# Kernel optimization log

Hardware: AMD Instinct MI355X
Metric: run time of the kernel (lower is better)

The kernel has to match this reference:

```python
import jax, jax.numpy as jnp
import numpy as np

B, T, D, H, L = 256, 128, 32, 512, 6
EPS = 1e-5


def setup_inputs() -> dict:
    key = jax.random.key(0)
    ks = jax.random.split(key, 12)
    sc = 0.02
    rn = lambda k, shp, s: (jax.random.normal(k, shp, jnp.float32) * s)
    return {
        "x": rn(ks[0], (B, T, D), 1.0),
        "w_proj": rn(ks[1], (H, D), sc),
        "b_proj": jnp.zeros((H,), jnp.float32),
        "w_ih": rn(ks[2], (L, 4 * H, H), sc),
        "w_hh": rn(ks[3], (L, 4 * H, H), sc),
        "b_ih": jnp.zeros((L, 4 * H), jnp.float32),
        "b_hh": jnp.zeros((L, 4 * H), jnp.float32),
        "ln_g": jnp.ones((L, H), jnp.float32),
        "ln_b": jnp.zeros((L, H), jnp.float32),
        "w1": rn(ks[4], (H, H), sc),
        "b1": jnp.zeros((H,), jnp.float32),
        "w2": rn(ks[5], (H // 2, H), sc),
        "b2": jnp.zeros((H // 2,), jnp.float32),
        "w3": rn(ks[6], (1, H // 2), sc),
        "b3": jnp.zeros((1,), jnp.float32),
    }


def _layer_norm(x, g, b):
    mu = jnp.mean(x, axis=-1, keepdims=True)
    var = jnp.mean(jnp.square(x - mu), axis=-1, keepdims=True)
    return (x - mu) * jax.lax.rsqrt(var + EPS) * g + b


def _lstm_layer(x, wih, whh, bih, bhh):
    # Precompute input-gate contributions for the whole sequence: [B,T,4H]
    xg = jnp.einsum("bth,gh->btg", x, wih) + (bih + bhh)
    h0 = jnp.zeros((x.shape[0], whh.shape[1]), x.dtype)

    def step(carry, xg_t):
        h, c = carry
        gates = xg_t + h @ whh.T  # [B,4H], torch gate order i,f,g,o
        i, f, g, o = jnp.split(gates, 4, axis=-1)
        i = jax.nn.sigmoid(i)
        f = jax.nn.sigmoid(f)
        g = jnp.tanh(g)
        o = jax.nn.sigmoid(o)
        c = f * c + i * g
        h = o * jnp.tanh(c)
        return (h, c), h

    _, hs = jax.lax.scan(step, (h0, h0), jnp.swapaxes(xg, 0, 1))  # hs: [T,B,H]
    return jnp.swapaxes(hs, 0, 1)  # [B,T,H]


def reference(x, w_proj, b_proj, w_ih, w_hh, b_ih, b_hh, ln_g, ln_b,
              w1, b1, w2, b2, w3, b3):
    h_prev = x @ w_proj.T + b_proj  # input projection: [B,T,H]
    for i in range(L):
        out = _lstm_layer(h_prev, w_ih[i], w_hh[i], b_ih[i], b_hh[i])
        out = _layer_norm(out, ln_g[i], ln_b[i])
        # dropout is identity in eval mode
        if i > 0:
            out = out + h_prev
        h_prev = out
    last = out[:, -1, :]  # [B,H]
    z = jax.nn.relu(last @ w1.T + b1)
    z = jax.nn.relu(z @ w2.T + b2)
    return z @ w3.T + b3  # [B,1]
```

## Files before the change

### kernel.cpp

```cpp
#include <hip/hip_runtime.h>
#include <hip/hip_bf16.h>
#include <stdint.h>

#define BB 256
#define TT 128
#define DD 32
#define HH 512
#define NL 6

typedef __attribute__((ext_vector_type(8))) short short8;
typedef __attribute__((ext_vector_type(4))) float f32x4;

__device__ __forceinline__ unsigned short f2bf(float f) {
    union { float f; unsigned u; } v; v.f = f;
    unsigned r = v.u + 0x7fff + ((v.u >> 16) & 1);
    return (unsigned short)(r >> 16);
}
__device__ __forceinline__ float bf2f(unsigned short s) {
    union { unsigned u; float f; } v; v.u = ((unsigned)s) << 16;
    return v.f;
}
__device__ __forceinline__ float fsig(float x) { return 1.0f / (1.0f + __expf(-x)); }
__device__ __forceinline__ float ftanh(float x) {
    float e = __expf(-2.0f * fabsf(x));
    float t = (1.0f - e) / (1.0f + e);
    return x < 0.0f ? -t : t;
}

__device__ __forceinline__ int4 g_load16_cc(const void* p) {
    int4 r;
    asm volatile("global_load_dwordx4 %0, %1, off sc0 sc1" : "=v"(r) : "v"(p) : "memory");
    return r;
}
__device__ __forceinline__ void g_store16_cc(void* p, int4 v) {
    union { int4 q; unsigned long long d[2]; } u; u.q = v;
    void* p2 = (void*)((char*)p + 8);
    asm volatile("global_store_dwordx2 %0, %1, off sc0 sc1" :: "v"(p), "v"(u.d[0]) : "memory");
    asm volatile("global_store_dwordx2 %0, %1, off sc0 sc1" :: "v"(p2), "v"(u.d[1]) : "memory");
}

__device__ __forceinline__ void poll_ge(unsigned int* p, unsigned target) {
    int guard = 0;
    while (__hip_atomic_load(p, __ATOMIC_RELAXED, __HIP_MEMORY_SCOPE_AGENT) < target &&
           ++guard < (1 << 17)) {}
}

__global__ __launch_bounds__(256) void k_zero(unsigned int* __restrict__ p, int n) {
    int i = blockIdx.x * 256 + threadIdx.x;
    if (i < n) p[i] = 0;
}

__global__ __launch_bounds__(256) void k_convert(const float* __restrict__ wih, const float* __restrict__ whh,
                                                 unsigned short* __restrict__ wih_bf, unsigned short* __restrict__ whh_bf,
                                                 int n4) {
    int i = blockIdx.x * 256 + threadIdx.x;
    if (i >= n4) return;
    float4 a = ((const float4*)wih)[i];
    float4 b = ((const float4*)whh)[i];
    ushort4 ra; ra.x = f2bf(a.x); ra.y = f2bf(a.y); ra.z = f2bf(a.z); ra.w = f2bf(a.w);
    ushort4 rb; rb.x = f2bf(b.x); rb.y = f2bf(b.y); rb.z = f2bf(b.z); rb.w = f2bf(b.w);
    ((ushort4*)wih_bf)[i] = ra;
    ((ushort4*)whh_bf)[i] = rb;
}

__global__ __launch_bounds__(512) void k_proj(const float* __restrict__ x, const float* __restrict__ wp,
                                              const float* __restrict__ bp,
                                              unsigned short* __restrict__ abf) {
    __shared__ float xs[64][DD];
    int m0 = blockIdx.x * 64;
    for (int i = threadIdx.x; i < 64 * DD; i += 512)
        xs[i >> 5][i & 31] = x[(size_t)(m0 + (i >> 5)) * DD + (i & 31)];
    __syncthreads();
    int n = threadIdx.x;
    float w[DD];
#pragma unroll
    for (int k = 0; k < DD; k++) w[k] = wp[n * DD + k];
    float bias = bp[n];
    for (int r = 0; r < 64; r++) {
        float acc = bias;
#pragma unroll
        for (int k = 0; k < DD; k++) acc += xs[r][k] * w[k];
        abf[(size_t)(m0 + r) * HH + n] = f2bf(acc);
    }
}

__device__ __forceinline__ void do_ln(int l, int tln, int row, int li, bool final_out,
                                      const unsigned short* __restrict__ hbuf,
                                      unsigned short* __restrict__ xring,
                                      const float* __restrict__ ln_g, const float* __restrict__ ln_b,
                                      float* __restrict__ xfinal) {
    const unsigned short* hrow = hbuf + ((size_t)(l * 2 + (tln & 1))) * 131072 + (size_t)row * 512 + li * 16;
    int4 h0 = g_load16_cc(hrow);
    int4 h1 = g_load16_cc(hrow + 8);
    int4 r0, r1;
    const bool res = (l > 0);
    if (res) {
        const unsigned short* xrow = xring + ((size_t)((l - 1) * 16 + (tln & 15))) * 131072 + (size_t)row * 512 + li * 16;
        r0 = g_load16_cc(xrow);
        r1 = g_load16_cc(xrow + 8);
    }
    asm volatile("s_waitcnt vmcnt(0)" ::: "memory");
    __builtin_amdgcn_sched_barrier(0);
    const unsigned short* hu0 = (const unsigned short*)&h0;
    const unsigned short* hu1 = (const unsigned short*)&h1;
    float v[16];
    float s = 0.f, ss = 0.f;
#pragma unroll
    for (int e = 0; e < 8; e++) { v[e] = bf2f(hu0[e]); v[e + 8] = bf2f(hu1[e]); }
#pragma unroll
    for (int e = 0; e < 16; e++) { s += v[e]; ss += v[e] * v[e]; }
#pragma unroll
    for (int off = 1; off < 32; off <<= 1) {
        s += __shfl_xor(s, off);
        ss += __shfl_xor(ss, off);
    }
    float mu = s * (1.f / 512.f);
    float var = ss * (1.f / 512.f) - mu * mu;
    float rs = rsqrtf(var + 1e-5f);
    const unsigned short* ru0 = (const unsigned short*)&r0;
    const unsigned short* ru1 = (const unsigned short*)&r1;
    float y[16];
#pragma unroll
    for (int e = 0; e < 16; e++) {
        float yy = (v[e] - mu) * rs * ln_g[l * 512 + li * 16 + e] + ln_b[l * 512 + li * 16 + e];
        if (res) yy += bf2f(e < 8 ? ru0[e] : ru1[e - 8]);
        y[e] = yy;
    }
    if (final_out) {
        float* dst = xfinal + (size_t)row * 512 + li * 16;
#pragma unroll
        for (int q = 0; q < 4; q++)
            *(float4*)(dst + q * 4) = (float4){y[q * 4], y[q * 4 + 1], y[q * 4 + 2], y[q * 4 + 3]};
    } else {
        unsigned short ys[16];
#pragma unroll
        for (int e = 0; e < 16; e++) ys[e] = f2bf(y[e]);
        unsigned short* dst = xring + ((size_t)(l * 16 + (tln & 15))) * 131072 + (size_t)row * 512 + li * 16;
        g_store16_cc(dst, *(int4*)&ys[0]);
        g_store16_cc(dst + 8, *(int4*)&ys[8]);
    }
}

__global__ __launch_bounds__(256, 1) void k_mega(
    const unsigned short* __restrict__ wih_bf,
    const unsigned short* __restrict__ whh_bf,
    const unsigned short* __restrict__ a_bf,
    const float* __restrict__ bih_all, const float* __restrict__ bhh_all,
    const float* __restrict__ ln_g, const float* __restrict__ ln_b,
    unsigned short* __restrict__ xring,
    unsigned short* __restrict__ hbuf,
    float* __restrict__ xfinal,
    unsigned int* __restrict__ cnt)
{
    __shared__ unsigned short smem[128 * 512];
    __shared__ unsigned short hstage[128 * 40];

    const int blk = blockIdx.x;
    const int l = blk >> 5;
    const int rr_ = blk & 31;
    const int g = rr_ >> 4;
    const int ui = rr_ & 15;
    const int tid = threadIdx.x, lane = tid & 63, w = tid >> 6;
    const int u0 = ui * 32;
    const int gb0 = g * 128;
    const int wb0 = gb0 + w * 32;
    const int uu = lane & 15;
    const int kg = lane >> 4;

    const unsigned short* wih = wih_bf + (size_t)l * 2048 * 512;
    const unsigned short* whh = whh_bf + (size_t)l * 2048 * 512;
    unsigned int* c1  = cnt + (l * 2 + g) * 64;
    unsigned int* c1n = cnt + ((l + 1) * 2 + g) * 64;
    unsigned int* c2  = cnt + (12 + l * 2 + g) * 64;
    unsigned int* c2u = cnt + (12 + (l - 1) * 2 + g) * 64;

    for (int c = tid; c < 128 * 64; c += 256) {
        int rr = c >> 6, k16 = c & 63;
        int grow = (rr >> 5) * 512 + u0 + ((rr >> 4) & 1) * 16 + (rr & 15);
        int4 v = *(const int4*)(whh + (size_t)grow * 512 + k16 * 8);
        int baddr = (rr * 1024 + k16 * 16) ^ ((rr & 7) << 4);
        *(int4*)((char*)smem + baddr) = v;
    }
    __syncthreads();

    float biasg[8];
#pragma unroll
    for (int rt = 0; rt < 8; rt++) {
        int grow = (rt >> 1) * 512 + u0 + ((rt & 1) << 4) + uu;
        biasg[rt] = bih_all[l * 2048 + grow] + bhh_all[l * 2048 + grow];
    }

    const int ln_row = gb0 + ui * 8 + w * 2 + (lane >> 5);
    const int li = lane & 31;
    f32x4 cst[4];
#pragma unroll
    for (int q = 0; q < 4; q++) cst[q] = (f32x4){0.f, 0.f, 0.f, 0.f};

#pragma unroll 1
    for (int t = 0; t < TT; ++t) {
        if (tid == 0) {
            if (t > 0) poll_ge(c1, 16u * (unsigned)t);
            if (l < 5 && t >= 17) poll_ge(c1n, 16u * (unsigned)(t - 15));
        }
        __syncthreads();

        if (t > 0 && l < 5) {
            do_ln(l, t - 1, ln_row, li, false, hbuf, xring, ln_g, ln_b, xfinal);
            asm volatile("s_waitcnt vmcnt(0)" ::: "memory");
            __syncthreads();
            if (tid == 0)
                __hip_atomic_fetch_add(c2, 1u, __ATOMIC_RELAXED, __HIP_MEMORY_SCOPE_AGENT);
        }

        if (l > 0) {
            if (tid == 0) poll_ge(c2u, 16u * (unsigned)(t + 1));
            __syncthreads();
        }

        f32x4 acc[2][8];
#pragma unroll
        for (int bt = 0; bt < 2; bt++)
#pragma unroll
            for (int rt = 0; rt < 8; rt++)
                acc[bt][rt] = (f32x4){biasg[rt], biasg[rt], biasg[rt], biasg[rt]};

#pragma unroll
        for (int half = 0; half < 2; half++) {
            short8 ax[2][8];
            if (l == 0) {
#pragma unroll
                for (int bt = 0; bt < 2; bt++)
#pragma unroll
                    for (int k8 = 0; k8 < 8; k8++)
                        ax[bt][k8] = *(const short8*)(a_bf + ((size_t)(wb0 + bt * 16 + uu) * TT + t) * 512 +
                                                      (half * 8 + k8) * 32 + kg * 8);
            } else {
                const unsigned short* xs = xring + ((size_t)((l - 1) * 16 + (t & 15))) * 131072;
                int4 ai[2][8];
#pragma unroll
                for (int bt = 0; bt < 2; bt++)
#pragma unroll
                    for (int k8 = 0; k8 < 8; k8++)
                        ai[bt][k8] = g_load16_cc(xs + (size_t)(wb0 + bt * 16 + uu) * 512 +
                                                 (half * 8 + k8) * 32 + kg * 8);
                asm volatile("s_waitcnt vmcnt(0)" ::: "memory");
                __builtin_amdgcn_sched_barrier(0);
#pragma unroll
                for (int bt = 0; bt < 2; bt++)
#pragma unroll
                    for (int k8 = 0; k8 < 8; k8++)
                        ax[bt][k8] = *(short8*)&ai[bt][k8];
            }
#pragma unroll
            for (int k8 = 0; k8 < 8; k8++) {
                int ks = half * 8 + k8;
#pragma unroll
                for (int rt = 0; rt < 8; rt++) {
                    short8 bfr = *(const short8*)(wih + (size_t)((rt >> 1) * 512 + u0 + ((rt & 1) << 4) + uu) * 512 +
                                                  ks * 32 + kg * 8);
                    acc[0][rt] = __builtin_amdgcn_mfma_f32_16x16x32_bf16(ax[0][k8], bfr, acc[0][rt], 0, 0, 0);
                    acc[1][rt] = __builtin_amdgcn_mfma_f32_16x16x32_bf16(ax[1][k8], bfr, acc[1][rt], 0, 0, 0);
                }
            }
        }

        if (t > 0) {
            const unsigned short* hp = hbuf + ((size_t)(l * 2 + ((t - 1) & 1))) * 131072;
#pragma unroll
            for (int half = 0; half < 2; half++) {
                int4 ai[2][8];
#pragma unroll
                for (int bt = 0; bt < 2; bt++)
#pragma unroll
                    for (int k8 = 0; k8 < 8; k8++)
                        ai[bt][k8] = g_load16_cc(hp + (size_t)(wb0 + bt * 16 + uu) * 512 +
                                                 (half * 8 + k8) * 32 + kg * 8);
                asm volatile("s_waitcnt vmcnt(0)" ::: "memory");
                __builtin_amdgcn_sched_barrier(0);
#pragma unroll
                for (int k8 = 0; k8 < 8; k8++) {
                    int k2 = ((half * 8 + k8) * 32 + kg * 8) * 2;
                    short8 ah0 = *(short8*)&ai[0][k8];
                    short8 ah1 = *(short8*)&ai[1][k8];
#pragma unroll
                    for (int rt = 0; rt < 8; rt++) {
                        int rr = rt * 16 + uu;
                        int baddr = (rr * 1024 + k2) ^ ((rr & 7) << 4);
                        short8 bh = *(const short8*)((const char*)smem + baddr);
                        acc[0][rt] = __builtin_amdgcn_mfma_f32_16x16x32_bf16(ah0, bh, acc[0][rt], 0, 0, 0);
                        acc[1][rt] = __builtin_amdgcn_mfma_f32_16x16x32_bf16(ah1, bh, acc[1][rt], 0, 0, 0);
                    }
                }
            }
        }

#pragma unroll
        for (int bt = 0; bt < 2; bt++)
#pragma unroll
            for (int usub = 0; usub < 2; usub++) {
                f32x4 iq = acc[bt][0 + usub], fq = acc[bt][2 + usub];
                f32x4 gq = acc[bt][4 + usub], oq = acc[bt][6 + usub];
#pragma unroll
                for (int j = 0; j < 4; j++) {
                    float i_ = fsig(iq[j]);
                    float f_ = fsig(fq[j]);
                    float g_ = ftanh(gq[j]);
                    float o_ = fsig(oq[j]);
                    float c = f_ * cst[bt * 2 + usub][j] + i_ * g_;
                    cst[bt * 2 + usub][j] = c;
                    float h = o_ * ftanh(c);
                    hstage[(w * 32 + bt * 16 + kg * 4 + j) * 40 + usub * 16 + uu] = f2bf(h);
                }
            }
        __syncthreads();
        {
            int lb = tid >> 1, hf = tid & 1;
            int4 v0 = *(const int4*)(hstage + lb * 40 + hf * 16);
            int4 v1 = *(const int4*)(hstage + lb * 40 + hf * 16 + 8);
            unsigned short* hd = hbuf + ((size_t)(l * 2 + (t & 1))) * 131072 + (size_t)(gb0 + lb) * 512 + u0 + hf * 16;
            g_store16_cc(hd, v0);
            g_store16_cc(hd + 8, v1);
        }
        asm volatile("s_waitcnt vmcnt(0)" ::: "memory");
        __syncthreads();
        if (tid == 0)
            __hip_atomic_fetch_add(c1, 1u, __ATOMIC_RELAXED, __HIP_MEMORY_SCOPE_AGENT);
    }

    if (tid == 0) poll_ge(c1, 16u * 128u);
    __syncthreads();
    if (l < 5) {
        do_ln(l, TT - 1, ln_row, li, false, hbuf, xring, ln_g, ln_b, xfinal);
        asm volatile("s_waitcnt vmcnt(0)" ::: "memory");
        __syncthreads();
        if (tid == 0)
            __hip_atomic_fetch_add(c2, 1u, __ATOMIC_RELAXED, __HIP_MEMORY_SCOPE_AGENT);
    } else {
        do_ln(l, TT - 1, ln_row, li, true, hbuf, xring, ln_g, ln_b, xfinal);
    }
}

__global__ __launch_bounds__(512) void k_mlp1(const float* __restrict__ xfinal, const float* __restrict__ w1,
                                              const float* __restrict__ b1, float* __restrict__ z1) {
    __shared__ float xs[512];
    int b = blockIdx.x;
    xs[threadIdx.x] = xfinal[(size_t)b * 512 + threadIdx.x];
    __syncthreads();
    int n = threadIdx.x;
    const float4* wr = (const float4*)(w1 + (size_t)n * 512);
    float acc = b1[n];
#pragma unroll 4
    for (int k4 = 0; k4 < 128; k4++) {
        float4 wv = wr[k4];
        acc += xs[k4 * 4 + 0] * wv.x + xs[k4 * 4 + 1] * wv.y + xs[k4 * 4 + 2] * wv.z + xs[k4 * 4 + 3] * wv.w;
    }
    z1[(size_t)b * 512 + n] = fmaxf(acc, 0.f);
}

__global__ __launch_bounds__(256) void k_mlp2(const float* __restrict__ z1, const float* __restrict__ w2,
                                              const float* __restrict__ b2, float* __restrict__ z2) {
    __shared__ float xs[512];
    int b = blockIdx.x;
    xs[threadIdx.x] = z1[(size_t)b * 512 + threadIdx.x];
    xs[threadIdx.x + 256] = z1[(size_t)b * 512 + threadIdx.x + 256];
    __syncthreads();
    int n = threadIdx.x;
    const float4* wr = (const float4*)(w2 + (size_t)n * 512);
    float acc = b2[n];
#pragma unroll 4
    for (int k4 = 0; k4 < 128; k4++) {
        float4 wv = wr[k4];
        acc += xs[k4 * 4 + 0] * wv.x + xs[k4 * 4 + 1] * wv.y + xs[k4 * 4 + 2] * wv.z + xs[k4 * 4 + 3] * wv.w;
    }
    z2[(size_t)b * 256 + n] = fmaxf(acc, 0.f);
}

__global__ __launch_bounds__(256) void k_mlp3(const float* __restrict__ z2, const float* __restrict__ w3,
                                              const float* __restrict__ b3, float* __restrict__ outp) {
    __shared__ float red[4];
    int b = blockIdx.x;
    int tid = threadIdx.x;
    float p = z2[(size_t)b * 256 + tid] * w3[tid];
#pragma unroll
    for (int off = 32; off > 0; off >>= 1) p += __shfl_down(p, off);
    if ((tid & 63) == 0) red[tid >> 6] = p;
    __syncthreads();
    if (tid == 0) outp[b] = red[0] + red[1] + red[2] + red[3] + b3[0];
}

extern "C" void kernel_launch(void* const* d_in, const int* in_sizes, int n_in,
                              void* d_out, int out_size, void* d_ws, size_t ws_size,
                              hipStream_t stream) {
    const float* x      = (const float*)d_in[0];
    const float* w_proj = (const float*)d_in[1];
    const float* b_proj = (const float*)d_in[2];
    const float* w_ih   = (const float*)d_in[3];
    const float* w_hh   = (const float*)d_in[4];
    const float* b_ih   = (const float*)d_in[5];
    const float* b_hh   = (const float*)d_in[6];
    const float* ln_g   = (const float*)d_in[7];
    const float* ln_b   = (const float*)d_in[8];
    const float* w1 = (const float*)d_in[9];  const float* b1 = (const float*)d_in[10];
    const float* w2 = (const float*)d_in[11]; const float* b2 = (const float*)d_in[12];
    const float* w3 = (const float*)d_in[13]; const float* b3 = (const float*)d_in[14];
    float* outp = (float*)d_out;

    char* ws = (char*)d_ws;
    size_t off = 0;
    auto alloc = [&](size_t sz) { char* p = ws + off; off += (sz + 255) & ~(size_t)255; return p; };
    unsigned short* a_bf   = (unsigned short*)alloc((size_t)32768 * 512 * 2);
    unsigned short* wih_bf = (unsigned short*)alloc((size_t)NL * 2048 * 512 * 2);
    unsigned short* whh_bf = (unsigned short*)alloc((size_t)NL * 2048 * 512 * 2);
    unsigned short* xring  = (unsigned short*)alloc((size_t)5 * 16 * 256 * 512 * 2);
    unsigned short* hbuf   = (unsigned short*)alloc((size_t)6 * 2 * 256 * 512 * 2);
    float*          xfinal = (float*)alloc((size_t)256 * 512 * 4);
    float*          z1     = (float*)alloc((size_t)256 * 512 * 4);
    float*          z2     = (float*)alloc((size_t)256 * 256 * 4);
    unsigned int*   cnt    = (unsigned int*)alloc(2048 * 4);

    k_zero<<<8, 256, 0, stream>>>(cnt, 2048);
    k_convert<<<6144, 256, 0, stream>>>(w_ih, w_hh, wih_bf, whh_bf, (NL * 2048 * 512) / 4);
    k_proj<<<512, 512, 0, stream>>>(x, w_proj, b_proj, a_bf);

    k_mega<<<192, 256, 0, stream>>>(wih_bf, whh_bf, a_bf, b_ih, b_hh, ln_g, ln_b,
                                    xring, hbuf, xfinal, cnt);

    k_mlp1<<<256, 512, 0, stream>>>(xfinal, w1, b1, z1);
    k_mlp2<<<256, 256, 0, stream>>>(z1, w2, b2, z2);
    k_mlp3<<<256, 256, 0, stream>>>(z2, w3, b3, outp);
}
```

Baseline: 9.298 ms.

## Store activations and hidden states in k-group-major tiled layout for coalesced loads

Changes the layout of the projected input, the inter-layer ring buffer and the hidden-state buffer from row-major [row][512] to a tiled [slot][kslice][kgroup][row][8] layout. The MFMA operand loads in the recurrent kernel, the LayerNorm loads/stores and the h-state stores are all rewritten to use it. The goal is to make the per-lane 16-byte loads of adjacent batch rows contiguous, so global and cache accesses on the latency-critical recurrent step coalesce better. The projection kernel now scatters its writes, and the LDS staging stride changes from 40 to 34, which may alter bank conflicts.

```diff
diff --git a/kernel.cpp b/kernel.cpp
--- a/kernel.cpp
+++ b/kernel.cpp
@@ -25,6 +25,10 @@
     float e = __expf(-2.0f * fabsf(x));
     float t = (1.0f - e) / (1.0f + e);
     return x < 0.0f ? -t : t;
+}
+
+__device__ __forceinline__ size_t xt_off(int slot, int ks, int kg, int row) {
+    return ((((size_t)slot * 16 + ks) * 4 + kg) * 256 + row) * 8;
 }
 
 __device__ __forceinline__ int4 g_load16_cc(const void* p) {
@@ -65,7 +69,7 @@
 
 __global__ __launch_bounds__(512) void k_proj(const float* __restrict__ x, const float* __restrict__ wp,
                                               const float* __restrict__ bp,
-                                              unsigned short* __restrict__ abf) {
+                                              unsigned short* __restrict__ abfT) {
     __shared__ float xs[64][DD];
     int m0 = blockIdx.x * 64;
     for (int i = threadIdx.x; i < 64 * DD; i += 512)
@@ -76,11 +80,14 @@
 #pragma unroll
     for (int k = 0; k < DD; k++) w[k] = wp[n * DD + k];
     float bias = bp[n];
+    const int ks = n >> 5, kg = (n >> 3) & 3, e = n & 7;
     for (int r = 0; r < 64; r++) {
         float acc = bias;
 #pragma unroll
         for (int k = 0; k < DD; k++) acc += xs[r][k] * w[k];
-        abf[(size_t)(m0 + r) * HH + n] = f2bf(acc);
+        int flat = m0 + r;
+        int b = flat >> 7, t = flat & 127;
+        abfT[xt_off(t, ks, kg, b) + e] = f2bf(acc);
     }
 }
 
@@ -89,15 +96,15 @@
                                       unsigned short* __restrict__ xring,
                                       const float* __restrict__ ln_g, const float* __restrict__ ln_b,
                                       float* __restrict__ xfinal) {
-    const unsigned short* hrow = hbuf + ((size_t)(l * 2 + (tln & 1))) * 131072 + (size_t)row * 512 + li * 16;
-    int4 h0 = g_load16_cc(hrow);
-    int4 h1 = g_load16_cc(hrow + 8);
+    const int ks = li >> 1, kgb = (li & 1) * 2;
+    int4 h0 = g_load16_cc(hbuf + xt_off(l * 2 + (tln & 1), ks, kgb, row));
+    int4 h1 = g_load16_cc(hbuf + xt_off(l * 2 + (tln & 1), ks, kgb + 1, row));
     int4 r0, r1;
     const bool res = (l > 0);
     if (res) {
-        const unsigned short* xrow = xring + ((size_t)((l - 1) * 16 + (tln & 15))) * 131072 + (size_t)row * 512 + li * 16;
-        r0 = g_load16_cc(xrow);
-        r1 = g_load16_cc(xrow + 8);
+        int slot = (l - 1) * 16 + (tln & 15);
+        r0 = g_load16_cc(xring + xt_off(slot, ks, kgb, row));
+        r1 = g_load16_cc(xring + xt_off(slot, ks, kgb + 1, row));
     }
     asm volatile("s_waitcnt vmcnt(0)" ::: "memory");
     __builtin_amdgcn_sched_barrier(0);
@@ -135,16 +142,16 @@
         unsigned short ys[16];
 #pragma unroll
         for (int e = 0; e < 16; e++) ys[e] = f2bf(y[e]);
-        unsigned short* dst = xring + ((size_t)(l * 16 + (tln & 15))) * 131072 + (size_t)row * 512 + li * 16;
-        g_store16_cc(dst, *(int4*)&ys[0]);
-        g_store16_cc(dst + 8, *(int4*)&ys[8]);
+        int slot = l * 16 + (tln & 15);
+        g_store16_cc(xring + xt_off(slot, ks, kgb, row), *(int4*)&ys[0]);
+        g_store16_cc(xring + xt_off(slot, ks, kgb + 1, row), *(int4*)&ys[8]);
     }
 }
 
 __global__ __launch_bounds__(256, 1) void k_mega(
     const unsigned short* __restrict__ wih_bf,
     const unsigned short* __restrict__ whh_bf,
-    const unsigned short* __restrict__ a_bf,
+    const unsigned short* __restrict__ a_bfT,
     const float* __restrict__ bih_all, const float* __restrict__ bhh_all,
     const float* __restrict__ ln_g, const float* __restrict__ ln_b,
     unsigned short* __restrict__ xring,
@@ -153,7 +160,7 @@
     unsigned int* __restrict__ cnt)
 {
     __shared__ unsigned short smem[128 * 512];
-    __shared__ unsigned short hstage[128 * 40];
+    __shared__ unsigned short hstage[128 * 34];
 
     const int blk = blockIdx.x;
     const int l = blk >> 5;
@@ -232,17 +239,15 @@
                 for (int bt = 0; bt < 2; bt++)
 #pragma unroll
                     for (int k8 = 0; k8 < 8; k8++)
-                        ax[bt][k8] = *(const short8*)(a_bf + ((size_t)(wb0 + bt * 16 + uu) * TT + t) * 512 +
-                                                      (half * 8 + k8) * 32 + kg * 8);
+                        ax[bt][k8] = *(const short8*)(a_bfT + xt_off(t, half * 8 + k8, kg, wb0 + bt * 16 + uu));
             } else {
-                const unsigned short* xs = xring + ((size_t)((l - 1) * 16 + (t & 15))) * 131072;
+                int slot = (l - 1) * 16 + (t & 15);
                 int4 ai[2][8];
 #pragma unroll
                 for (int bt = 0; bt < 2; bt++)
 #pragma unroll
                     for (int k8 = 0; k8 < 8; k8++)
-                        ai[bt][k8] = g_load16_cc(xs + (size_t)(wb0 + bt * 16 + uu) * 512 +
-                                                 (half * 8 + k8) * 32 + kg * 8);
+                        ai[bt][k8] = g_load16_cc(xring + xt_off(slot, half * 8 + k8, kg, wb0 + bt * 16 + uu));
                 asm volatile("s_waitcnt vmcnt(0)" ::: "memory");
                 __builtin_amdgcn_sched_barrier(0);
 #pragma unroll
@@ -265,7 +270,7 @@
         }
 
         if (t > 0) {
-            const unsigned short* hp = hbuf + ((size_t)(l * 2 + ((t - 1) & 1))) * 131072;
+            const int hslot = l * 2 + ((t - 1) & 1);
 #pragma unroll
             for (int half = 0; half < 2; half++) {
                 int4 ai[2][8];
@@ -273,8 +278,7 @@
                 for (int bt = 0; bt < 2; bt++)
 #pragma unroll
                     for (int k8 = 0; k8 < 8; k8++)
-                        ai[bt][k8] = g_load16_cc(hp + (size_t)(wb0 + bt * 16 + uu) * 512 +
-                                                 (half * 8 + k8) * 32 + kg * 8);
+                        ai[bt][k8] = g_load16_cc(hbuf + xt_off(hslot, half * 8 + k8, kg, wb0 + bt * 16 + uu));
                 asm volatile("s_waitcnt vmcnt(0)" ::: "memory");
                 __builtin_amdgcn_sched_barrier(0);
 #pragma unroll
@@ -309,17 +313,19 @@
                     float c = f_ * cst[bt * 2 + usub][j] + i_ * g_;
                     cst[bt * 2 + usub][j] = c;
                     float h = o_ * ftanh(c);
-                    hstage[(w * 32 + bt * 16 + kg * 4 + j) * 40 + usub * 16 + uu] = f2bf(h);
+                    hstage[(w * 32 + bt * 16 + kg * 4 + j) * 34 + usub * 16 + uu] = f2bf(h);
                 }
             }
         __syncthreads();
         {
-            int lb = tid >> 1, hf = tid & 1;
-            int4 v0 = *(const int4*)(hstage + lb * 40 + hf * 16);
-            int4 v1 = *(const int4*)(hstage + lb * 40 + hf * 16 + 8);
-            unsigned short* hd = hbuf + ((size_t)(l * 2 + (t & 1))) * 131072 + (size_t)(gb0 + lb) * 512 + u0 + hf * 16;
-            g_store16_cc(hd, v0);
-            g_store16_cc(hd + 8, v1);
+            const int hdst = l * 2 + (t & 1);
+#pragma unroll
+            for (int c = 0; c < 2; c++) {
+                int idx = c * 256 + tid;
+                int kgp = idx >> 7, rowp = idx & 127;
+                int4 v = *(const int4*)(hstage + rowp * 34 + kgp * 8);
+                g_store16_cc(hbuf + xt_off(hdst, ui, kgp, gb0 + rowp), v);
+            }
         }
         asm volatile("s_waitcnt vmcnt(0)" ::: "memory");
         __syncthreads();
@@ -408,11 +414,11 @@
     char* ws = (char*)d_ws;
     size_t off = 0;
     auto alloc = [&](size_t sz) { char* p = ws + off; off += (sz + 255) & ~(size_t)255; return p; };
-    unsigned short* a_bf   = (unsigned short*)alloc((size_t)32768 * 512 * 2);
+    unsigned short* a_bfT  = (unsigned short*)alloc((size_t)128 * 131072 * 2);
     unsigned short* wih_bf = (unsigned short*)alloc((size_t)NL * 2048 * 512 * 2);
     unsigned short* whh_bf = (unsigned short*)alloc((size_t)NL * 2048 * 512 * 2);
-    unsigned short* xring  = (unsigned short*)alloc((size_t)5 * 16 * 256 * 512 * 2);
-    unsigned short* hbuf   = (unsigned short*)alloc((size_t)6 * 2 * 256 * 512 * 2);
+    unsigned short* xring  = (unsigned short*)alloc((size_t)80 * 131072 * 2);
+    unsigned short* hbuf   = (unsigned short*)alloc((size_t)12 * 131072 * 2);
     float*          xfinal = (float*)alloc((size_t)256 * 512 * 4);
     float*          z1     = (float*)alloc((size_t)256 * 512 * 4);
     float*          z2     = (float*)alloc((size_t)256 * 256 * 4);
@@ -420,9 +426,9 @@
 
     k_zero<<<8, 256, 0, stream>>>(cnt, 2048);
     k_convert<<<6144, 256, 0, stream>>>(w_ih, w_hh, wih_bf, whh_bf, (NL * 2048 * 512) / 4);
-    k_proj<<<512, 512, 0, stream>>>(x, w_proj, b_proj, a_bf);
-
-    k_mega<<<192, 256, 0, stream>>>(wih_bf, whh_bf, a_bf, b_ih, b_hh, ln_g, ln_b,
+    k_proj<<<512, 512, 0, stream>>>(x, w_proj, b_proj, a_bfT);
+
+    k_mega<<<192, 256, 0, stream>>>(wih_bf, whh_bf, a_bfT, b_ih, b_hh, ln_g, ln_b,
                                     xring, hbuf, xfinal, cnt);
 
     k_mlp1<<<256, 512, 0, stream>>>(xfinal, w1, b1, z1);
```

New measurement: 9.014 ms. -3.1%, faster.
